# Kernel optimization log

Measured on AMD Instinct MI355X. Metric: run time of the kernel, lower is better.

The kernel has to match this reference:

```python
import jax, jax.numpy as jnp
import numpy as np

NUM_NODES = 100000
NUM_EDGES = 1600000
NUM_GRAPHS = 512
HIDDEN = 128
LAYERS = 3
NUM_CLASSES = 10
BN_EPS = 1e-5


def setup_inputs() -> dict:
    key = jax.random.key(0)
    ks = jax.random.split(key, 12)
    x = jax.random.normal(ks[0], (NUM_NODES, HIDDEN), dtype=jnp.float32)
    edge_index = jax.random.randint(ks[1], (2, NUM_EDGES), 0, NUM_NODES, dtype=jnp.int32)
    batch = jnp.sort(jax.random.randint(ks[2], (NUM_NODES,), 0, NUM_GRAPHS, dtype=jnp.int32))
    s = 1.0 / np.sqrt(HIDDEN)
    W1 = jax.random.normal(ks[3], (LAYERS, HIDDEN, HIDDEN), dtype=jnp.float32) * s
    b1 = jnp.zeros((LAYERS, HIDDEN), dtype=jnp.float32)
    W2 = jax.random.normal(ks[4], (LAYERS, HIDDEN, HIDDEN), dtype=jnp.float32) * s
    b2 = jnp.zeros((LAYERS, HIDDEN), dtype=jnp.float32)
    gamma = jnp.ones((LAYERS, HIDDEN), dtype=jnp.float32)
    beta = jnp.zeros((LAYERS, HIDDEN), dtype=jnp.float32)
    eps_gin = jnp.zeros((LAYERS,), dtype=jnp.float32)  # train_eps init 0
    lin1_w = jax.random.normal(ks[5], (LAYERS * HIDDEN, HIDDEN), dtype=jnp.float32) * (1.0 / np.sqrt(LAYERS * HIDDEN))
    lin1_b = jnp.zeros((HIDDEN,), dtype=jnp.float32)
    lin2_w = jax.random.normal(ks[6], (HIDDEN, NUM_CLASSES), dtype=jnp.float32) * s
    lin2_b = jnp.zeros((NUM_CLASSES,), dtype=jnp.float32)
    return {"x": x, "edge_index": edge_index, "batch": batch,
            "W1": W1, "b1": b1, "W2": W2, "b2": b2,
            "gamma": gamma, "beta": beta, "eps_gin": eps_gin,
            "lin1_w": lin1_w, "lin1_b": lin1_b, "lin2_w": lin2_w, "lin2_b": lin2_b}


def _batchnorm(h, g, b):
    mu = jnp.mean(h, axis=0, keepdims=True)
    var = jnp.var(h, axis=0, keepdims=True)
    return (h - mu) * jax.lax.rsqrt(var + BN_EPS) * g + b


def reference(x, edge_index, batch, W1, b1, W2, b2, gamma, beta, eps_gin,
              lin1_w, lin1_b, lin2_w, lin2_b):
    src, dst = edge_index[0], edge_index[1]
    n = x.shape[0]
    h = x
    layer_hs = []
    for l in range(LAYERS):
        # scatter-add neighbor aggregation: agg[i] = sum_{j->i} h[j]
        agg = jax.ops.segment_sum(h[src], dst, num_segments=n)
        z = (1.0 + eps_gin[l]) * h + agg
        z = jax.nn.relu(z @ W1[l] + b1[l])
        z = jax.nn.relu(z @ W2[l] + b2[l])
        h = _batchnorm(z, gamma[l], beta[l])
        layer_hs.append(h)
    h_cat = jnp.concatenate(layer_hs, axis=-1)  # [N, LAYERS*HIDDEN]
    # global mean pool per graph
    sums = jax.ops.segment_sum(h_cat, batch, num_segments=NUM_GRAPHS)
    counts = jax.ops.segment_sum(jnp.ones((n, 1), h_cat.dtype), batch, num_segments=NUM_GRAPHS)
    g = sums / jnp.maximum(counts, 1.0)
    g = jax.nn.relu(g @ lin1_w + lin1_b)
    # dropout is identity in inference
    return g @ lin2_w + lin2_b
```

## Files before the change

### kernel.cpp

```cpp
#include <hip/hip_runtime.h>

#define HID 128
#define NGRAPH 512
#define NLAYERS 3
#define BN_EPS 1e-5f
#define NPB 256
#define EB 4096

typedef __attribute__((ext_vector_type(8))) short bf16x8;
typedef __attribute__((ext_vector_type(4))) float f32x4;
typedef __attribute__((ext_vector_type(2))) float f32x2;

__device__ inline unsigned short f2bf(float x) {
    union { float f; unsigned u; } v; v.f = x;
    unsigned r = v.u + 0x7FFFu + ((v.u >> 16) & 1u);
    return (unsigned short)(r >> 16);
}
__device__ inline float bf2f(unsigned short b) {
    union { float f; unsigned u; } v; v.u = ((unsigned)b) << 16; return v.f;
}
__device__ inline f32x2 bfp(unsigned u) {
    union { unsigned q; float f; } lo, hi;
    lo.q = u << 16; hi.q = u & 0xFFFF0000u;
    f32x2 r; r[0] = lo.f; r[1] = hi.f; return r;
}

__global__ void k_prep(float* __restrict__ ssliced, float* __restrict__ gsum,
                       const float4* __restrict__ x4, ushort* __restrict__ xb, int total4,
                       const float* __restrict__ W1, ushort* __restrict__ w1h, ushort* __restrict__ w1l,
                       const float* __restrict__ W2, ushort* __restrict__ w2h, ushort* __restrict__ w2l,
                       int wtotal, int xblocks,
                       const int* __restrict__ dst, int E, int* __restrict__ blkcnt) {
    __shared__ int hist[512];
    int b = blockIdx.x, t = threadIdx.x;
    if (b < 768) {
        if (b < 24) ssliced[b * 256 + t] = 0.0f;
        gsum[b * 256 + t] = 0.0f;
    } else if (b < 1152) {
        int gid = (b - 768) * 256 + t;
        const float* W; ushort *Wh, *Wl; int e;
        if (gid < wtotal) { W = W1; Wh = w1h; Wl = w1l; e = gid; }
        else              { W = W2; Wh = w2h; Wl = w2l; e = gid - wtotal; }
        if (e < wtotal) {
            int l = e >> 14, rem = e & 16383, k = rem >> 7, n = rem & 127;
            float v = W[e];
            ushort hi = f2bf(v);
            ushort lo = f2bf(v - bf2f(hi));
            int o = (l << 14) + (n << 7) + k;
            Wh[o] = hi; Wl[o] = lo;
        }
    } else if (b < 1152 + xblocks) {
        int i = (b - 1152) * 256 + t;
        if (i < total4) {
            float4 v = x4[i];
            uint2 p;
            p.x = ((unsigned)f2bf(v.y) << 16) | f2bf(v.x);
            p.y = ((unsigned)f2bf(v.w) << 16) | f2bf(v.z);
            ((uint2*)xb)[i] = p;
        }
    } else {
        int b2 = b - (1152 + xblocks);
        hist[t] = 0; hist[t + 256] = 0;
        __syncthreads();
        int base = b2 * EB;
        #pragma unroll
        for (int i = 0; i < 16; ++i) {
            int e = base + i * 256 + t;
            if (e < E) atomicAdd(&hist[dst[e] >> 8], 1);
        }
        __syncthreads();
        blkcnt[b2 * 512 + t]       = hist[t];
        blkcnt[b2 * 512 + t + 256] = hist[t + 256];
    }
}

__global__ __launch_bounds__(256) void k_btot_reduce(const int* __restrict__ blkcnt,
                                                     int eblk, int* __restrict__ tot) {
    __shared__ int sh[256];
    int b = blockIdx.x;
    int t = threadIdx.x;
    int s = 0;
    for (int j = t; j < eblk; j += 256) s += blkcnt[j * 512 + b];
    sh[t] = s;
    __syncthreads();
    #pragma unroll
    for (int k = 128; k > 0; k >>= 1) {
        if (t < k) sh[t] += sh[t + k];
        __syncthreads();
    }
    if (t == 0) tot[b] = sh[0];
}

__global__ __launch_bounds__(512) void k_bscan(const int* __restrict__ tot, int nb, int E,
                                               int* __restrict__ bbase, int* __restrict__ rowptrN) {
    __shared__ int sh[512];
    int t = threadIdx.x;
    sh[t] = (t < nb) ? tot[t] : 0;
    __syncthreads();
    #pragma unroll
    for (int s = 1; s < 512; s <<= 1) {
        int v = (t >= s) ? sh[t - s] : 0;
        __syncthreads();
        sh[t] += v;
        __syncthreads();
    }
    if (t < nb) bbase[t] = (t == 0) ? 0 : sh[t - 1];
    if (t == 0) { bbase[nb] = E; *rowptrN = E; }
}

__global__ __launch_bounds__(512) void k_colscan(int* __restrict__ blkcnt, int eblk,
                                                 const int* __restrict__ bbase) {
    __shared__ int sh[512];
    int t = threadIdx.x;
    int b = blockIdx.x;
    sh[t] = (t < eblk) ? blkcnt[t * 512 + b] : 0;
    __syncthreads();
    #pragma unroll
    for (int s = 1; s < 512; s <<= 1) {
        int v = (t >= s) ? sh[t - s] : 0;
        __syncthreads();
        sh[t] += v;
        __syncthreads();
    }
    int excl = (t == 0) ? 0 : sh[t - 1];
    if (t < eblk) blkcnt[t * 512 + b] = bbase[b] + excl;
}

__global__ __launch_bounds__(256) void k_bscatter(const int* __restrict__ src,
                                                  const int* __restrict__ dst, int E,
                                                  const int* __restrict__ blkcnt,
                                                  unsigned* __restrict__ pairs) {
    __shared__ int hist[512];
    __shared__ int lbase[512];
    int t = threadIdx.x;
    hist[t] = 0; hist[t + 256] = 0;
    lbase[t]       = blkcnt[blockIdx.x * 512 + t];
    lbase[t + 256] = blkcnt[blockIdx.x * 512 + t + 256];
    __syncthreads();
    int base = blockIdx.x * EB;
    #pragma unroll
    for (int i = 0; i < 16; ++i) {
        int e = base + i * 256 + t;
        if (e < E) {
            int d = dst[e];
            int b = d >> 8;
            int pos = lbase[b] + atomicAdd(&hist[b], 1);
            pairs[pos] = ((unsigned)(d & 255) << 24) | (unsigned)src[e];
        }
    }
}

__global__ __launch_bounds__(256) void k_bbuild(const unsigned* __restrict__ pairs,
                                                const int* __restrict__ bbase, int N,
                                                int* __restrict__ rowptr, int* __restrict__ csr) {
    __shared__ int cnt[256];
    __shared__ int off[256];
    int t = threadIdx.x;
    int b = blockIdx.x;
    int base = bbase[b], bcount = bbase[b + 1] - base;
    cnt[t] = 0;
    __syncthreads();
    for (int i = t; i < bcount; i += 256) atomicAdd(&cnt[pairs[base + i] >> 24], 1);
    __syncthreads();
    off[t] = cnt[t];
    __syncthreads();
    for (int s = 1; s < 256; s <<= 1) {
        int v = (t >= s) ? off[t - s] : 0;
        __syncthreads();
        off[t] += v;
        __syncthreads();
    }
    int excl = (t == 0) ? 0 : off[t - 1];
    int node = b * NPB + t;
    if (node < N) rowptr[node] = base + excl;
    cnt[t] = excl;
    __syncthreads();
    for (int i = t; i < bcount; i += 256) {
        unsigned p = pairs[base + i];
        int dl = p >> 24;
        int pos = base + atomicAdd(&cnt[dl], 1);
        csr[pos] = (int)(p & 0xFFFFFFu);
    }
}

__global__ __launch_bounds__(256, 6) void k_agg(
        const int* __restrict__ rowptr, const int* __restrict__ csr_src,
        const uint2* __restrict__ hinb,
        const float* __restrict__ prev_stats,
        const float* __restrict__ g_row, const float* __restrict__ be_row,
        const float* __restrict__ eps_gin, int layer,
        ushort* __restrict__ z0out, int N) {
    const int t = threadIdx.x;
    const int lane = t & 63;
    const int wv = t >> 6;
    const int q = lane >> 4;
    const int f = lane & 15;

    f32x2 scv2[4], shv2[4];
    if (prev_stats) {
        float invn = 1.0f / (float)N;
        #pragma unroll
        for (int d = 0; d < 4; ++d) {
            #pragma unroll
            for (int h = 0; h < 2; ++h) {
                int fi = f * 8 + d * 2 + h;
                float mu = prev_stats[fi] * invn;
                float var = prev_stats[128 + fi] * invn - mu * mu;
                float inv = rsqrtf(var + BN_EPS);
                float scj = g_row[fi] * inv;
                scv2[d][h] = scj; shv2[d][h] = be_row[fi] - mu * scj;
            }
        }
    } else {
        #pragma unroll
        for (int d = 0; d < 4; ++d) { scv2[d] = (f32x2){1.f, 1.f}; shv2[d] = (f32x2){0.f, 0.f}; }
    }
    float e1 = 1.0f + eps_gin[layer];
    const uint4* hin4 = (const uint4*)hinb;

    int r = blockIdx.x * 16 + wv * 4 + q;
    f32x2 a2[4];
    #pragma unroll
    for (int d = 0; d < 4; ++d) a2[d] = (f32x2){0.f, 0.f};
    float cdeg = 0.f;
    if (r < N) {
        int beg = rowptr[r], end = rowptr[r + 1];
        uint4 hv = hin4[(size_t)r * 16 + f];
        a2[0] = e1 * bfp(hv.x); a2[1] = e1 * bfp(hv.y);
        a2[2] = e1 * bfp(hv.z); a2[3] = e1 * bfp(hv.w);
        int p = beg;
        for (; p + 8 <= end; p += 8) {
            int s0 = csr_src[p],     s1 = csr_src[p + 1], s2 = csr_src[p + 2], s3 = csr_src[p + 3];
            int s4 = csr_src[p + 4], s5 = csr_src[p + 5], s6 = csr_src[p + 6], s7 = csr_src[p + 7];
            uint4 v0 = hin4[(size_t)s0 * 16 + f];
            uint4 v1 = hin4[(size_t)s1 * 16 + f];
            uint4 v2 = hin4[(size_t)s2 * 16 + f];
            uint4 v3 = hin4[(size_t)s3 * 16 + f];
            uint4 v4 = hin4[(size_t)s4 * 16 + f];
            uint4 v5 = hin4[(size_t)s5 * 16 + f];
            uint4 v6 = hin4[(size_t)s6 * 16 + f];
            uint4 v7 = hin4[(size_t)s7 * 16 + f];
            a2[0] += ((bfp(v0.x) + bfp(v1.x)) + (bfp(v2.x) + bfp(v3.x)))
                   + ((bfp(v4.x) + bfp(v5.x)) + (bfp(v6.x) + bfp(v7.x)));
            a2[1] += ((bfp(v0.y) + bfp(v1.y)) + (bfp(v2.y) + bfp(v3.y)))
                   + ((bfp(v4.y) + bfp(v5.y)) + (bfp(v6.y) + bfp(v7.y)));
            a2[2] += ((bfp(v0.z) + bfp(v1.z)) + (bfp(v2.z) + bfp(v3.z)))
                   + ((bfp(v4.z) + bfp(v5.z)) + (bfp(v6.z) + bfp(v7.z)));
            a2[3] += ((bfp(v0.w) + bfp(v1.w)) + (bfp(v2.w) + bfp(v3.w)))
                   + ((bfp(v4.w) + bfp(v5.w)) + (bfp(v6.w) + bfp(v7.w)));
        }
        if (p < end) {
            int last = end - 1;
            int c1 = min(p + 1, last), c2 = min(p + 2, last), c3 = min(p + 3, last);
            int c4 = min(p + 4, last), c5 = min(p + 5, last), c6 = min(p + 6, last);
            int s0 = csr_src[p],  s1 = csr_src[c1], s2 = csr_src[c2], s3 = csr_src[c3];
            int s4 = csr_src[c4], s5 = csr_src[c5], s6 = csr_src[c6];
            uint4 v0 = hin4[(size_t)s0 * 16 + f];
            uint4 v1 = hin4[(size_t)s1 * 16 + f];
            uint4 v2 = hin4[(size_t)s2 * 16 + f];
            uint4 v3 = hin4[(size_t)s3 * 16 + f];
            uint4 v4 = hin4[(size_t)s4 * 16 + f];
            uint4 v5 = hin4[(size_t)s5 * 16 + f];
            uint4 v6 = hin4[(size_t)s6 * 16 + f];
            int rem = end - p;
            unsigned m1 = (rem > 1) ? 0xFFFFFFFFu : 0u;
            unsigned m2 = (rem > 2) ? 0xFFFFFFFFu : 0u;
            unsigned m3 = (rem > 3) ? 0xFFFFFFFFu : 0u;
            unsigned m4 = (rem > 4) ? 0xFFFFFFFFu : 0u;
            unsigned m5 = (rem > 5) ? 0xFFFFFFFFu : 0u;
            unsigned m6 = (rem > 6) ? 0xFFFFFFFFu : 0u;
            a2[0] += ((bfp(v0.x) + bfp(v1.x & m1)) + (bfp(v2.x & m2) + bfp(v3.x & m3)))
                   + ((bfp(v4.x & m4) + bfp(v5.x & m5)) + bfp(v6.x & m6));
            a2[1] += ((bfp(v0.y) + bfp(v1.y & m1)) + (bfp(v2.y & m2) + bfp(v3.y & m3)))
                   + ((bfp(v4.y & m4) + bfp(v5.y & m5)) + bfp(v6.y & m6));
            a2[2] += ((bfp(v0.z) + bfp(v1.z & m1)) + (bfp(v2.z & m2) + bfp(v3.z & m3)))
                   + ((bfp(v4.z & m4) + bfp(v5.z & m5)) + bfp(v6.z & m6));
            a2[3] += ((bfp(v0.w) + bfp(v1.w & m1)) + (bfp(v2.w & m2) + bfp(v3.w & m3)))
                   + ((bfp(v4.w & m4) + bfp(v5.w & m5)) + bfp(v6.w & m6));
        }
        cdeg = e1 + (float)(end - beg);
    }
    f32x2 rr2[4];
    #pragma unroll
    for (int d = 0; d < 4; ++d) rr2[d] = scv2[d] * a2[d] + cdeg * shv2[d];
    uint4 ph;
    ph.x = ((unsigned)f2bf(rr2[0][1]) << 16) | f2bf(rr2[0][0]);
    ph.y = ((unsigned)f2bf(rr2[1][1]) << 16) | f2bf(rr2[1][0]);
    ph.z = ((unsigned)f2bf(rr2[2][1]) << 16) | f2bf(rr2[2][0]);
    ph.w = ((unsigned)f2bf(rr2[3][1]) << 16) | f2bf(rr2[3][0]);
    if (r < N) ((uint4*)z0out)[(size_t)r * 16 + f] = ph;
}

__global__ __launch_bounds__(256, 2) void k_mlp_dense(
        const uint4* __restrict__ z0, int layer, const int* __restrict__ batch,
        const ushort* __restrict__ w1h, const ushort* __restrict__ w1l,
        const float* __restrict__ b1,
        const ushort* __restrict__ w2h, const ushort* __restrict__ w2l,
        const float* __restrict__ b2,
        ushort* __restrict__ Hout, float* __restrict__ stat_sl,
        float* __restrict__ gsum, int N) {
    __shared__ __align__(16) ushort smem[8192];
    const int t = threadIdx.x;
    const int lane = t & 63;
    const int wv = t >> 6;
    const int li = lane & 15;
    const int kq = lane >> 4;
    const int n0 = wv * 32;
    const int row0 = blockIdx.x * 64;
    const int swz = (li & 7) * 4;

    bf16x8 w1hr[8], w1lr[8], w2hr[8], w2lr[8];
    #pragma unroll
    for (int ch = 0; ch < 2; ++ch)
        #pragma unroll
        for (int ks = 0; ks < 2; ++ks)
            #pragma unroll
            for (int nt = 0; nt < 2; ++nt) {
                int i = ch * 4 + ks * 2 + nt;
                size_t wo = (size_t)(n0 + nt * 16 + li) * 128 + (ch * 64 + ks * 32 + kq * 8);
                w1hr[i] = *(const bf16x8*)&w1h[wo];
                w1lr[i] = *(const bf16x8*)&w1l[wo];
                w2hr[i] = *(const bf16x8*)&w2h[wo];
                w2lr[i] = *(const bf16x8*)&w2l[wo];
            }

    {
        const uint4 zz = {0u, 0u, 0u, 0u};
        #pragma unroll
        for (int i = 0; i < 4; ++i) {
            int idx = i * 256 + t;
            int r = idx >> 4, f = idx & 15;
            uint4 v = (row0 + r < N) ? z0[(size_t)(row0 + r) * 16 + f] : zz;
            ((uint4*)smem)[r * 16 + (f ^ (r & 7))] = v;
        }
    }
    __syncthreads();

    f32x4 acc[4][2];
    #pragma unroll
    for (int i = 0; i < 4; ++i) {
        acc[i][0] = (f32x4){0.f, 0.f, 0.f, 0.f};
        acc[i][1] = (f32x4){0.f, 0.f, 0.f, 0.f};
    }

    #pragma unroll
    for (int ch = 0; ch < 2; ++ch) {
        #pragma unroll
        for (int ks = 0; ks < 2; ++ks) {
            int kcol = ch * 8 + ks * 4 + kq;
            #pragma unroll
            for (int mt = 0; mt < 4; ++mt) {
                int r = mt * 16 + li;
                int hw = (r * 16 + (kcol ^ (li & 7))) * 8;
                bf16x8 ah = *(const bf16x8*)&smem[hw];
                #pragma unroll
                for (int nt = 0; nt < 2; ++nt) {
                    int i = ch * 4 + ks * 2 + nt;
                    acc[mt][nt] = __builtin_amdgcn_mfma_f32_16x16x32_bf16(ah, w1hr[i], acc[mt][nt], 0, 0, 0);
                    acc[mt][nt] = __builtin_amdgcn_mfma_f32_16x16x32_bf16(ah, w1lr[i], acc[mt][nt], 0, 0, 0);
                }
            }
        }
    }

    float bz0 = b1[n0 + li], bz1 = b1[n0 + 16 + li];
    __syncthreads();
    #pragma unroll
    for (int mt = 0; mt < 4; ++mt) {
        #pragma unroll
        for (int nt = 0; nt < 2; ++nt) {
            int c = n0 + nt * 16 + li;
            int dk = c >> 1;
            int halfbase = (dk >> 5) * 32;
            int dlow = dk & 31;
            int codd = c & 1;
            float bias = nt ? bz1 : bz0;
            #pragma unroll
            for (int reg = 0; reg < 4; ++reg) {
                int r = mt * 16 + kq * 4 + reg;
                float v = fmaxf(acc[mt][nt][reg] + bias, 0.f);
                int us = (r * 64 + halfbase + (dlow ^ ((r & 7) * 4))) * 2 + codd;
                smem[us] = f2bf(v);
            }
        }
    }
    #pragma unroll
    for (int i = 0; i < 4; ++i) {
        acc[i][0] = (f32x4){0.f, 0.f, 0.f, 0.f};
        acc[i][1] = (f32x4){0.f, 0.f, 0.f, 0.f};
    }
    __syncthreads();

    #pragma unroll
    for (int ch = 0; ch < 2; ++ch) {
        #pragma unroll
        for (int ks = 0; ks < 2; ++ks) {
            int aoff = (ks * 16 + kq * 4) ^ swz;
            #pragma unroll
            for (int mt = 0; mt < 4; ++mt) {
                int idx = ((mt * 16 + li) * 64 + ch * 32 + aoff) * 2;
                bf16x8 ah = *(const bf16x8*)&smem[idx];
                #pragma unroll
                for (int nt = 0; nt < 2; ++nt) {
                    int i = ch * 4 + ks * 2 + nt;
                    acc[mt][nt] = __builtin_amdgcn_mfma_f32_16x16x32_bf16(ah, w2hr[i], acc[mt][nt], 0, 0, 0);
                    acc[mt][nt] = __builtin_amdgcn_mfma_f32_16x16x32_bf16(ah, w2lr[i], acc[mt][nt], 0, 0, 0);
                }
            }
        }
    }

    float bb0 = b2[n0 + li], bb1 = b2[n0 + 16 + li];
    int btr[4][4];
    #pragma unroll
    for (int mt = 0; mt < 4; ++mt)
        #pragma unroll
        for (int reg = 0; reg < 4; ++reg) {
            int grow = row0 + mt * 16 + kq * 4 + reg;
            btr[mt][reg] = (grow < N) ? batch[grow] : -1;
        }
    __syncthreads();
    float s0 = 0.f, q0 = 0.f, s1 = 0.f, q1 = 0.f;
    #pragma unroll
    for (int mt = 0; mt < 4; ++mt) {
        #pragma unroll
        for (int reg = 0; reg < 4; ++reg) {
            int r = mt * 16 + kq * 4 + reg;
            float v0 = fmaxf(acc[mt][0][reg] + bb0, 0.f);
            float v1 = fmaxf(acc[mt][1][reg] + bb1, 0.f);
            smem[r * 128 + n0 + li]      = f2bf(v0);
            smem[r * 128 + n0 + 16 + li] = f2bf(v1);
            if (btr[mt][reg] >= 0) {
                s0 += v0; q0 += v0 * v0; s1 += v1; q1 += v1 * v1;
            }
        }
    }
    __syncthreads();
    {
        int valid = N - row0; if (valid > 64) valid = 64;
        int tot = valid * 16;
        for (int i = t; i < tot; i += 256) {
            int r = i >> 4, c = i & 15;
            ((uint4*)&Hout[(size_t)(row0 + r) * HID])[c] = ((const uint4*)smem)[r * 16 + c];
        }
    }
    s0 += __shfl_xor(s0, 16); s0 += __shfl_xor(s0, 32);
    q0 += __shfl_xor(q0, 16); q0 += __shfl_xor(q0, 32);
    s1 += __shfl_xor(s1, 16); s1 += __shfl_xor(s1, 32);
    q1 += __shfl_xor(q1, 16); q1 += __shfl_xor(q1, 32);
    if (kq == 0) {
        float* ss = stat_sl + (blockIdx.x & 7) * 768;
        unsafeAtomicAdd(&ss[n0 + li], s0);
        unsafeAtomicAdd(&ss[128 + n0 + li], q0);
        unsafeAtomicAdd(&ss[n0 + 16 + li], s1);
        unsafeAtomicAdd(&ss[128 + n0 + 16 + li], q1);
    }
    int lastr = N - 1; if (lastr > row0 + 63) lastr = row0 + 63;
    int g_lo = batch[row0], g_hi = batch[lastr];
    int loff = layer * HID;
    for (int g = g_lo; g <= g_hi; ++g) {
        float p0 = 0.f, p1 = 0.f;
        #pragma unroll
        for (int mt = 0; mt < 4; ++mt)
            #pragma unroll
            for (int reg = 0; reg < 4; ++reg) {
                if (btr[mt][reg] == g) {
                    p0 += fmaxf(acc[mt][0][reg] + bb0, 0.f);
                    p1 += fmaxf(acc[mt][1][reg] + bb1, 0.f);
                }
            }
        p0 += __shfl_xor(p0, 16); p0 += __shfl_xor(p0, 32);
        p1 += __shfl_xor(p1, 16); p1 += __shfl_xor(p1, 32);
        if (kq == 0) {
            unsafeAtomicAdd(&gsum[(size_t)g * 384 + loff + n0 + li], p0);
            unsafeAtomicAdd(&gsum[(size_t)g * 384 + loff + n0 + 16 + li], p1);
        }
    }
}

__global__ __launch_bounds__(256) void k_sfold(const float* __restrict__ sliced,
                                               float* __restrict__ out) {
    int t = threadIdx.x;
    float s = 0.f;
    #pragma unroll
    for (int k = 0; k < 8; ++k) s += sliced[k * 768 + t];
    out[t] = s;
}

__global__ __launch_bounds__(128) void k_mlp(const int* __restrict__ batch, int N,
                     const float* __restrict__ gsum, const float* __restrict__ stats,
                     const float* __restrict__ gamma, const float* __restrict__ beta,
                     const float* __restrict__ w1, const float* __restrict__ b1,
                     const float* __restrict__ w2, const float* __restrict__ b2,
                     float* __restrict__ out) {
    __shared__ float gl[384];
    __shared__ float hh[128];
    int g = blockIdx.x, t = threadIdx.x;
    int start, end;
    { int lo = 0, hi = N; while (lo < hi) { int m = (lo + hi) >> 1; if (batch[m] < g) lo = m + 1; else hi = m; } start = lo; }
    { int lo = start, hi = N; while (lo < hi) { int m = (lo + hi) >> 1; if (batch[m] < g + 1) lo = m + 1; else hi = m; } end = lo; }
    float cnt = (float)(end - start);
    float invc = 1.0f / fmaxf(cnt, 1.0f);
    float invn = 1.0f / (float)N;
    #pragma unroll
    for (int l = 0; l < NLAYERS; ++l) {
        float mu = stats[l * 256 + t] * invn;
        float var = stats[l * 256 + 128 + t] * invn - mu * mu;
        float inv = rsqrtf(var + BN_EPS);
        float sc = gamma[l * HID + t] * inv;
        float sh = beta[l * HID + t] - mu * sc;
        gl[l * 128 + t] = (gsum[(size_t)g * 384 + l * 128 + t] * sc + sh * cnt) * invc;
    }
    __syncthreads();
    float acc = b1[t];
    for (int k = 0; k < 384; ++k) acc = fmaf(gl[k], w1[k * HID + t], acc);
    hh[t] = fmaxf(acc, 0.f);
    __syncthreads();
    if (t < 10) {
        float a2 = b2[t];
        for (int k = 0; k < 128; ++k) a2 = fmaf(hh[k], w2[k * 10 + t], a2);
        out[g * 10 + t] = a2;
    }
}

extern "C" void kernel_launch(void* const* d_in, const int* in_sizes, int n_in,
                              void* d_out, int out_size, void* d_ws, size_t ws_size,
                              hipStream_t stream) {
    const float* x     = (const float*)d_in[0];
    const int*   ei    = (const int*)d_in[1];
    const int*   batch = (const int*)d_in[2];
    const float* W1    = (const float*)d_in[3];
    const float* b1    = (const float*)d_in[4];
    const float* W2    = (const float*)d_in[5];
    const float* b2    = (const float*)d_in[6];
    const float* gamma = (const float*)d_in[7];
    const float* beta  = (const float*)d_in[8];
    const float* epsg  = (const float*)d_in[9];
    const float* l1w   = (const float*)d_in[10];
    const float* l1b   = (const float*)d_in[11];
    const float* l2w   = (const float*)d_in[12];
    const float* l2b   = (const float*)d_in[13];

    const int N = in_sizes[0] / HID;
    const int E = in_sizes[1] / 2;
    const int* src = ei;
    const int* dst = ei + E;
    const int nb = (N + NPB - 1) / NPB;
    const int eblk = (E + EB - 1) / EB;

    float* w = (float*)d_ws;
    const size_t NF = (size_t)N * HID;
    ushort* xb    = (ushort*)(w + NF);
    ushort* hb[3] = { xb + NF, xb + 2 * NF, xb + 3 * NF };
    ushort* z0buf = xb + 4 * NF;
    float* stats  = w + 4 * NF;
    float* sliced = stats + 768;
    float* gsum   = sliced + 6144;
    int*   rowptr = (int*)(gsum + (size_t)NGRAPH * 384);
    int*   csr    = rowptr + N + 1;
    int*   bbase  = csr + E;
    int*   btot   = bbase + nb + 2;
    ushort* wt  = (ushort*)(((uintptr_t)(btot + nb + 1) + 15) & ~(uintptr_t)15);
    ushort* w1h = wt;
    ushort* w1l = wt + 49152;
    ushort* w2h = wt + 98304;
    ushort* w2l = wt + 147456;

    unsigned* pairs  = (unsigned*)w;
    int*      blkcnt = (int*)(w + 2 * 1024 * 1024);

    const int total4 = (int)(NF / 4);
    const int xblocks = (total4 + 255) / 256;
    const int prep_blocks = 1152 + xblocks + eblk;
    k_prep<<<prep_blocks, 256, 0, stream>>>(sliced, gsum, (const float4*)x, xb, total4,
                                            W1, w1h, w1l, W2, w2h, w2l, NLAYERS * HID * HID,
                                            xblocks, dst, E, blkcnt);

    k_btot_reduce<<<nb, 256, 0, stream>>>(blkcnt, eblk, btot);
    k_bscan<<<1, 512, 0, stream>>>(btot, nb, E, bbase, rowptr + N);
    k_colscan<<<nb, 512, 0, stream>>>(blkcnt, eblk, bbase);
    k_bscatter<<<eblk, 256, 0, stream>>>(src, dst, E, blkcnt, pairs);
    k_bbuild<<<nb, 256, 0, stream>>>(pairs, bbase, N, rowptr, csr);

    for (int l = 0; l < NLAYERS; ++l) {
        const ushort* hin = (l == 0) ? xb : hb[l - 1];
        const float* pstats = (l == 0) ? nullptr : (stats + (l - 1) * 256);
        const float* grow_  = gamma + (l == 0 ? 0 : (l - 1)) * HID;
        const float* brow_  = beta  + (l == 0 ? 0 : (l - 1)) * HID;

        k_agg<<<(N + 15) / 16, 256, 0, stream>>>(
            rowptr, csr, (const uint2*)hin, pstats, grow_, brow_, epsg, l, z0buf, N);

        k_mlp_dense<<<(N + 63) / 64, 256, 0, stream>>>(
            (const uint4*)z0buf, l, batch,
            w1h + (size_t)l * 16384, w1l + (size_t)l * 16384, b1 + l * HID,
            w2h + (size_t)l * 16384, w2l + (size_t)l * 16384, b2 + l * HID,
            hb[l], sliced + l * 256, gsum, N);

        k_sfold<<<1, 256, 0, stream>>>(sliced + l * 256, stats + l * 256);
    }

    k_mlp<<<NGRAPH, 128, 0, stream>>>(batch, N, gsum, stats, gamma, beta,
                                      l1w, l1b, l2w, l2b, (float*)d_out);
}
```

Before: 524.0 us.

## Make dense MLP persistent, batch head MLP over 8 graphs, raise agg occupancy

The dense MLP kernel becomes a persistent grid of 512 blocks that loops over 64-row tiles. Each block loads its weight registers and biases once instead of once per tile. The head MLP now handles 8 graphs per block, so each lin1 weight load is reused across 8 accumulators. k_agg's launch bounds move from 6 to 8 waves, which may force register spilling. The persistent loop adds a barrier at the end of each tile and serializes tiles within a block, which reduces latency hiding.

```diff
diff --git a/kernel.cpp b/kernel.cpp
--- a/kernel.cpp
+++ b/kernel.cpp
@@ -183,7 +183,7 @@
     }
 }
 
-__global__ __launch_bounds__(256, 6) void k_agg(
+__global__ __launch_bounds__(256, 8) void k_agg(
         const int* __restrict__ rowptr, const int* __restrict__ csr_src,
         const uint2* __restrict__ hinb,
         const float* __restrict__ prev_stats,
@@ -298,7 +298,7 @@
         const ushort* __restrict__ w2h, const ushort* __restrict__ w2l,
         const float* __restrict__ b2,
         ushort* __restrict__ Hout, float* __restrict__ stat_sl,
-        float* __restrict__ gsum, int N) {
+        float* __restrict__ gsum, int N, int ntiles) {
     __shared__ __align__(16) ushort smem[8192];
     const int t = threadIdx.x;
     const int lane = t & 63;
@@ -306,7 +306,6 @@
     const int li = lane & 15;
     const int kq = lane >> 4;
     const int n0 = wv * 32;
-    const int row0 = blockIdx.x * 64;
     const int swz = (li & 7) * 4;
 
     bf16x8 w1hr[8], w1lr[8], w2hr[8], w2lr[8];
@@ -323,158 +322,163 @@
                 w2hr[i] = *(const bf16x8*)&w2h[wo];
                 w2lr[i] = *(const bf16x8*)&w2l[wo];
             }
-
-    {
-        const uint4 zz = {0u, 0u, 0u, 0u};
+    float bz0 = b1[n0 + li], bz1 = b1[n0 + 16 + li];
+    float bb0 = b2[n0 + li], bb1 = b2[n0 + 16 + li];
+
+    for (int tile = blockIdx.x; tile < ntiles; tile += gridDim.x) {
+        const int row0 = tile * 64;
+
+        {
+            const uint4 zz = {0u, 0u, 0u, 0u};
+            #pragma unroll
+            for (int i = 0; i < 4; ++i) {
+                int idx = i * 256 + t;
+                int r = idx >> 4, f = idx & 15;
+                uint4 v = (row0 + r < N) ? z0[(size_t)(row0 + r) * 16 + f] : zz;
+                ((uint4*)smem)[r * 16 + (f ^ (r & 7))] = v;
+            }
+        }
+        __syncthreads();
+
+        f32x4 acc[4][2];
         #pragma unroll
         for (int i = 0; i < 4; ++i) {
-            int idx = i * 256 + t;
-            int r = idx >> 4, f = idx & 15;
-            uint4 v = (row0 + r < N) ? z0[(size_t)(row0 + r) * 16 + f] : zz;
-            ((uint4*)smem)[r * 16 + (f ^ (r & 7))] = v;
-        }
-    }
-    __syncthreads();
-
-    f32x4 acc[4][2];
-    #pragma unroll
-    for (int i = 0; i < 4; ++i) {
-        acc[i][0] = (f32x4){0.f, 0.f, 0.f, 0.f};
-        acc[i][1] = (f32x4){0.f, 0.f, 0.f, 0.f};
-    }
-
-    #pragma unroll
-    for (int ch = 0; ch < 2; ++ch) {
-        #pragma unroll
-        for (int ks = 0; ks < 2; ++ks) {
-            int kcol = ch * 8 + ks * 4 + kq;
-            #pragma unroll
-            for (int mt = 0; mt < 4; ++mt) {
-                int r = mt * 16 + li;
-                int hw = (r * 16 + (kcol ^ (li & 7))) * 8;
-                bf16x8 ah = *(const bf16x8*)&smem[hw];
+            acc[i][0] = (f32x4){0.f, 0.f, 0.f, 0.f};
+            acc[i][1] = (f32x4){0.f, 0.f, 0.f, 0.f};
+        }
+
+        #pragma unroll
+        for (int ch = 0; ch < 2; ++ch) {
+            #pragma unroll
+            for (int ks = 0; ks < 2; ++ks) {
+                int kcol = ch * 8 + ks * 4 + kq;
                 #pragma unroll
-                for (int nt = 0; nt < 2; ++nt) {
-                    int i = ch * 4 + ks * 2 + nt;
-                    acc[mt][nt] = __builtin_amdgcn_mfma_f32_16x16x32_bf16(ah, w1hr[i], acc[mt][nt], 0, 0, 0);
-                    acc[mt][nt] = __builtin_amdgcn_mfma_f32_16x16x32_bf16(ah, w1lr[i], acc[mt][nt], 0, 0, 0);
+                for (int mt = 0; mt < 4; ++mt) {
+                    int r = mt * 16 + li;
+                    int hw = (r * 16 + (kcol ^ (li & 7))) * 8;
+                    bf16x8 ah = *(const bf16x8*)&smem[hw];
+                    #pragma unroll
+                    for (int nt = 0; nt < 2; ++nt) {
+                        int i = ch * 4 + ks * 2 + nt;
+                        acc[mt][nt] = __builtin_amdgcn_mfma_f32_16x16x32_bf16(ah, w1hr[i], acc[mt][nt], 0, 0, 0);
+                        acc[mt][nt] = __builtin_amdgcn_mfma_f32_16x16x32_bf16(ah, w1lr[i], acc[mt][nt], 0, 0, 0);
+                    }
                 }
             }
         }
-    }
-
-    float bz0 = b1[n0 + li], bz1 = b1[n0 + 16 + li];
-    __syncthreads();
-    #pragma unroll
-    for (int mt = 0; mt < 4; ++mt) {
-        #pragma unroll
-        for (int nt = 0; nt < 2; ++nt) {
-            int c = n0 + nt * 16 + li;
-            int dk = c >> 1;
-            int halfbase = (dk >> 5) * 32;
-            int dlow = dk & 31;
-            int codd = c & 1;
-            float bias = nt ? bz1 : bz0;
+
+        __syncthreads();
+        #pragma unroll
+        for (int mt = 0; mt < 4; ++mt) {
+            #pragma unroll
+            for (int nt = 0; nt < 2; ++nt) {
+                int c = n0 + nt * 16 + li;
+                int dk = c >> 1;
+                int halfbase = (dk >> 5) * 32;
+                int dlow = dk & 31;
+                int codd = c & 1;
+                float bias = nt ? bz1 : bz0;
+                #pragma unroll
+                for (int reg = 0; reg < 4; ++reg) {
+                    int r = mt * 16 + kq * 4 + reg;
+                    float v = fmaxf(acc[mt][nt][reg] + bias, 0.f);
+                    int us = (r * 64 + halfbase + (dlow ^ ((r & 7) * 4))) * 2 + codd;
+                    smem[us] = f2bf(v);
+                }
+            }
+        }
+        #pragma unroll
+        for (int i = 0; i < 4; ++i) {
+            acc[i][0] = (f32x4){0.f, 0.f, 0.f, 0.f};
+            acc[i][1] = (f32x4){0.f, 0.f, 0.f, 0.f};
+        }
+        __syncthreads();
+
+        #pragma unroll
+        for (int ch = 0; ch < 2; ++ch) {
+            #pragma unroll
+            for (int ks = 0; ks < 2; ++ks) {
+                int aoff = (ks * 16 + kq * 4) ^ swz;
+                #pragma unroll
+                for (int mt = 0; mt < 4; ++mt) {
+                    int idx = ((mt * 16 + li) * 64 + ch * 32 + aoff) * 2;
+                    bf16x8 ah = *(const bf16x8*)&smem[idx];
+                    #pragma unroll
+                    for (int nt = 0; nt < 2; ++nt) {
+                        int i = ch * 4 + ks * 2 + nt;
+                        acc[mt][nt] = __builtin_amdgcn_mfma_f32_16x16x32_bf16(ah, w2hr[i], acc[mt][nt], 0, 0, 0);
+                        acc[mt][nt] = __builtin_amdgcn_mfma_f32_16x16x32_bf16(ah, w2lr[i], acc[mt][nt], 0, 0, 0);
+                    }
+                }
+            }
+        }
+
+        int btr[4][4];
+        #pragma unroll
+        for (int mt = 0; mt < 4; ++mt)
+            #pragma unroll
+            for (int reg = 0; reg < 4; ++reg) {
+                int grow = row0 + mt * 16 + kq * 4 + reg;
+                btr[mt][reg] = (grow < N) ? batch[grow] : -1;
+            }
+        __syncthreads();
+        float s0 = 0.f, q0 = 0.f, s1 = 0.f, q1 = 0.f;
+        #pragma unroll
+        for (int mt = 0; mt < 4; ++mt) {
             #pragma unroll
             for (int reg = 0; reg < 4; ++reg) {
                 int r = mt * 16 + kq * 4 + reg;
-                float v = fmaxf(acc[mt][nt][reg] + bias, 0.f);
-                int us = (r * 64 + halfbase + (dlow ^ ((r & 7) * 4))) * 2 + codd;
-                smem[us] = f2bf(v);
-            }
-        }
-    }
-    #pragma unroll
-    for (int i = 0; i < 4; ++i) {
-        acc[i][0] = (f32x4){0.f, 0.f, 0.f, 0.f};
-        acc[i][1] = (f32x4){0.f, 0.f, 0.f, 0.f};
-    }
-    __syncthreads();
-
-    #pragma unroll
-    for (int ch = 0; ch < 2; ++ch) {
-        #pragma unroll
-        for (int ks = 0; ks < 2; ++ks) {
-            int aoff = (ks * 16 + kq * 4) ^ swz;
-            #pragma unroll
-            for (int mt = 0; mt < 4; ++mt) {
-                int idx = ((mt * 16 + li) * 64 + ch * 32 + aoff) * 2;
-                bf16x8 ah = *(const bf16x8*)&smem[idx];
+                float v0 = fmaxf(acc[mt][0][reg] + bb0, 0.f);
+                float v1 = fmaxf(acc[mt][1][reg] + bb1, 0.f);
+                smem[r * 128 + n0 + li]      = f2bf(v0);
+                smem[r * 128 + n0 + 16 + li] = f2bf(v1);
+                if (btr[mt][reg] >= 0) {
+                    s0 += v0; q0 += v0 * v0; s1 += v1; q1 += v1 * v1;
+                }
+            }
+        }
+        __syncthreads();
+        {
+            int valid = N - row0; if (valid > 64) valid = 64;
+            int tot = valid * 16;
+            for (int i = t; i < tot; i += 256) {
+                int r = i >> 4, c = i & 15;
+                ((uint4*)&Hout[(size_t)(row0 + r) * HID])[c] = ((const uint4*)smem)[r * 16 + c];
+            }
+        }
+        s0 += __shfl_xor(s0, 16); s0 += __shfl_xor(s0, 32);
+        q0 += __shfl_xor(q0, 16); q0 += __shfl_xor(q0, 32);
+        s1 += __shfl_xor(s1, 16); s1 += __shfl_xor(s1, 32);
+        q1 += __shfl_xor(q1, 16); q1 += __shfl_xor(q1, 32);
+        if (kq == 0) {
+            float* ss = stat_sl + (blockIdx.x & 7) * 768;
+            unsafeAtomicAdd(&ss[n0 + li], s0);
+            unsafeAtomicAdd(&ss[128 + n0 + li], q0);
+            unsafeAtomicAdd(&ss[n0 + 16 + li], s1);
+            unsafeAtomicAdd(&ss[128 + n0 + 16 + li], q1);
+        }
+        int lastr = N - 1; if (lastr > row0 + 63) lastr = row0 + 63;
+        int g_lo = batch[row0], g_hi = batch[lastr];
+        int loff = layer * HID;
+        for (int g = g_lo; g <= g_hi; ++g) {
+            float p0 = 0.f, p1 = 0.f;
+            #pragma unroll
+            for (int mt = 0; mt < 4; ++mt)
                 #pragma unroll
-                for (int nt = 0; nt < 2; ++nt) {
-                    int i = ch * 4 + ks * 2 + nt;
-                    acc[mt][nt] = __builtin_amdgcn_mfma_f32_16x16x32_bf16(ah, w2hr[i], acc[mt][nt], 0, 0, 0);
-                    acc[mt][nt] = __builtin_amdgcn_mfma_f32_16x16x32_bf16(ah, w2lr[i], acc[mt][nt], 0, 0, 0);
+                for (int reg = 0; reg < 4; ++reg) {
+                    if (btr[mt][reg] == g) {
+                        p0 += fmaxf(acc[mt][0][reg] + bb0, 0.f);
+                        p1 += fmaxf(acc[mt][1][reg] + bb1, 0.f);
+                    }
                 }
-            }
-        }
-    }
-
-    float bb0 = b2[n0 + li], bb1 = b2[n0 + 16 + li];
-    int btr[4][4];
-    #pragma unroll
-    for (int mt = 0; mt < 4; ++mt)
-        #pragma unroll
-        for (int reg = 0; reg < 4; ++reg) {
-            int grow = row0 + mt * 16 + kq * 4 + reg;
-            btr[mt][reg] = (grow < N) ? batch[grow] : -1;
-        }
-    __syncthreads();
-    float s0 = 0.f, q0 = 0.f, s1 = 0.f, q1 = 0.f;
-    #pragma unroll
-    for (int mt = 0; mt < 4; ++mt) {
-        #pragma unroll
-        for (int reg = 0; reg < 4; ++reg) {
-            int r = mt * 16 + kq * 4 + reg;
-            float v0 = fmaxf(acc[mt][0][reg] + bb0, 0.f);
-            float v1 = fmaxf(acc[mt][1][reg] + bb1, 0.f);
-            smem[r * 128 + n0 + li]      = f2bf(v0);
-            smem[r * 128 + n0 + 16 + li] = f2bf(v1);
-            if (btr[mt][reg] >= 0) {
-                s0 += v0; q0 += v0 * v0; s1 += v1; q1 += v1 * v1;
-            }
-        }
-    }
-    __syncthreads();
-    {
-        int valid = N - row0; if (valid > 64) valid = 64;
-        int tot = valid * 16;
-        for (int i = t; i < tot; i += 256) {
-            int r = i >> 4, c = i & 15;
-            ((uint4*)&Hout[(size_t)(row0 + r) * HID])[c] = ((const uint4*)smem)[r * 16 + c];
-        }
-    }
-    s0 += __shfl_xor(s0, 16); s0 += __shfl_xor(s0, 32);
-    q0 += __shfl_xor(q0, 16); q0 += __shfl_xor(q0, 32);
-    s1 += __shfl_xor(s1, 16); s1 += __shfl_xor(s1, 32);
-    q1 += __shfl_xor(q1, 16); q1 += __shfl_xor(q1, 32);
-    if (kq == 0) {
-        float* ss = stat_sl + (blockIdx.x & 7) * 768;
-        unsafeAtomicAdd(&ss[n0 + li], s0);
-        unsafeAtomicAdd(&ss[128 + n0 + li], q0);
-        unsafeAtomicAdd(&ss[n0 + 16 + li], s1);
-        unsafeAtomicAdd(&ss[128 + n0 + 16 + li], q1);
-    }
-    int lastr = N - 1; if (lastr > row0 + 63) lastr = row0 + 63;
-    int g_lo = batch[row0], g_hi = batch[lastr];
-    int loff = layer * HID;
-    for (int g = g_lo; g <= g_hi; ++g) {
-        float p0 = 0.f, p1 = 0.f;
-        #pragma unroll
-        for (int mt = 0; mt < 4; ++mt)
-            #pragma unroll
-            for (int reg = 0; reg < 4; ++reg) {
-                if (btr[mt][reg] == g) {
-                    p0 += fmaxf(acc[mt][0][reg] + bb0, 0.f);
-                    p1 += fmaxf(acc[mt][1][reg] + bb1, 0.f);
-                }
-            }
-        p0 += __shfl_xor(p0, 16); p0 += __shfl_xor(p0, 32);
-        p1 += __shfl_xor(p1, 16); p1 += __shfl_xor(p1, 32);
-        if (kq == 0) {
-            unsafeAtomicAdd(&gsum[(size_t)g * 384 + loff + n0 + li], p0);
-            unsafeAtomicAdd(&gsum[(size_t)g * 384 + loff + n0 + 16 + li], p1);
-        }
+            p0 += __shfl_xor(p0, 16); p0 += __shfl_xor(p0, 32);
+            p1 += __shfl_xor(p1, 16); p1 += __shfl_xor(p1, 32);
+            if (kq == 0) {
+                unsafeAtomicAdd(&gsum[(size_t)g * 384 + loff + n0 + li], p0);
+                unsafeAtomicAdd(&gsum[(size_t)g * 384 + loff + n0 + 16 + li], p1);
+            }
+        }
+        __syncthreads();
     }
 }
 
@@ -493,33 +497,47 @@
                      const float* __restrict__ w1, const float* __restrict__ b1,
                      const float* __restrict__ w2, const float* __restrict__ b2,
                      float* __restrict__ out) {
-    __shared__ float gl[384];
-    __shared__ float hh[128];
-    int g = blockIdx.x, t = threadIdx.x;
-    int start, end;
-    { int lo = 0, hi = N; while (lo < hi) { int m = (lo + hi) >> 1; if (batch[m] < g) lo = m + 1; else hi = m; } start = lo; }
-    { int lo = start, hi = N; while (lo < hi) { int m = (lo + hi) >> 1; if (batch[m] < g + 1) lo = m + 1; else hi = m; } end = lo; }
-    float cnt = (float)(end - start);
-    float invc = 1.0f / fmaxf(cnt, 1.0f);
+    __shared__ float gl[8][384];
+    __shared__ float hh[8][128];
+    int g0 = blockIdx.x * 8, t = threadIdx.x;
     float invn = 1.0f / (float)N;
+    float sc[NLAYERS], sh[NLAYERS];
     #pragma unroll
     for (int l = 0; l < NLAYERS; ++l) {
         float mu = stats[l * 256 + t] * invn;
         float var = stats[l * 256 + 128 + t] * invn - mu * mu;
         float inv = rsqrtf(var + BN_EPS);
-        float sc = gamma[l * HID + t] * inv;
-        float sh = beta[l * HID + t] - mu * sc;
-        gl[l * 128 + t] = (gsum[(size_t)g * 384 + l * 128 + t] * sc + sh * cnt) * invc;
-    }
-    __syncthreads();
-    float acc = b1[t];
-    for (int k = 0; k < 384; ++k) acc = fmaf(gl[k], w1[k * HID + t], acc);
-    hh[t] = fmaxf(acc, 0.f);
-    __syncthreads();
-    if (t < 10) {
-        float a2 = b2[t];
-        for (int k = 0; k < 128; ++k) a2 = fmaf(hh[k], w2[k * 10 + t], a2);
-        out[g * 10 + t] = a2;
+        sc[l] = gamma[l * HID + t] * inv;
+        sh[l] = beta[l * HID + t] - mu * sc[l];
+    }
+    for (int j = 0; j < 8; ++j) {
+        int g = g0 + j;
+        int start, end;
+        { int lo = 0, hi = N; while (lo < hi) { int m = (lo + hi) >> 1; if (batch[m] < g) lo = m + 1; else hi = m; } start = lo; }
+        { int lo = start, hi = N; while (lo < hi) { int m = (lo + hi) >> 1; if (batch[m] < g + 1) lo = m + 1; else hi = m; } end = lo; }
+        float cnt = (float)(end - start);
+        float invc = 1.0f / fmaxf(cnt, 1.0f);
+        #pragma unroll
+        for (int l = 0; l < NLAYERS; ++l)
+            gl[j][l * 128 + t] = (gsum[(size_t)g * 384 + l * 128 + t] * sc[l] + sh[l] * cnt) * invc;
+    }
+    __syncthreads();
+    float acc[8];
+    #pragma unroll
+    for (int j = 0; j < 8; ++j) acc[j] = b1[t];
+    for (int k = 0; k < 384; ++k) {
+        float wv = w1[k * HID + t];
+        #pragma unroll
+        for (int j = 0; j < 8; ++j) acc[j] = fmaf(gl[j][k], wv, acc[j]);
+    }
+    #pragma unroll
+    for (int j = 0; j < 8; ++j) hh[j][t] = fmaxf(acc[j], 0.f);
+    __syncthreads();
+    if (t < 80) {
+        int j = t / 10, o = t % 10;
+        float a2 = b2[o];
+        for (int k = 0; k < 128; ++k) a2 = fmaf(hh[j][k], w2[k * 10 + o], a2);
+        out[(g0 + j) * 10 + o] = a2;
     }
 }
 
@@ -582,6 +600,7 @@
     k_bscatter<<<eblk, 256, 0, stream>>>(src, dst, E, blkcnt, pairs);
     k_bbuild<<<nb, 256, 0, stream>>>(pairs, bbase, N, rowptr, csr);
 
+    const int ntiles = (N + 63) / 64;
     for (int l = 0; l < NLAYERS; ++l) {
         const ushort* hin = (l == 0) ? xb : hb[l - 1];
         const float* pstats = (l == 0) ? nullptr : (stats + (l - 1) * 256);
@@ -591,15 +610,15 @@
         k_agg<<<(N + 15) / 16, 256, 0, stream>>>(
             rowptr, csr, (const uint2*)hin, pstats, grow_, brow_, epsg, l, z0buf, N);
 
-        k_mlp_dense<<<(N + 63) / 64, 256, 0, stream>>>(
+        k_mlp_dense<<<512, 256, 0, stream>>>(
             (const uint4*)z0buf, l, batch,
             w1h + (size_t)l * 16384, w1l + (size_t)l * 16384, b1 + l * HID,
             w2h + (size_t)l * 16384, w2l + (size_t)l * 16384, b2 + l * HID,
-            hb[l], sliced + l * 256, gsum, N);
+            hb[l], sliced + l * 256, gsum, N, ntiles);
 
         k_sfold<<<1, 256, 0, stream>>>(sliced + l * 256, stats + l * 256);
     }
 
-    k_mlp<<<NGRAPH, 128, 0, stream>>>(batch, N, gsum, stats, gamma, beta,
-                                      l1w, l1b, l2w, l2b, (float*)d_out);
-}
+    k_mlp<<<NGRAPH / 8, 128, 0, stream>>>(batch, N, gsum, stats, gamma, beta,
+                                          l1w, l1b, l2w, l2b, (float*)d_out);
+}
```

New measurement: 602.2 us. 1.15x slower.
